# Kernel optimization log

Hardware: AMD Instinct MI355X
Metric: run time of the kernel (lower is better)

Reference implementation:

```python
import jax, jax.numpy as jnp
import numpy as np

DT = 0.1


def setup_inputs() -> dict:
    key = jax.random.key(0)
    k1, k2, k3, k4 = jax.random.split(key, 4)
    B, T, I, H, O = 32, 1024, 256, 512, 256
    return {
        "x": jax.random.normal(k1, (B, T, I), dtype=jnp.float32),
        "input_weights": jax.random.normal(k2, (H, I), dtype=jnp.float32) * (1.0 / np.sqrt(I)),
        "recurrent_weights": jax.random.normal(k3, (H, H), dtype=jnp.float32) * (1.0 / np.sqrt(H)),
        "time_constants": jnp.ones((H,), dtype=jnp.float32) + 0.1,
        "output_weights": jax.random.normal(k4, (O, H), dtype=jnp.float32) * (1.0 / np.sqrt(H)),
        "bias": jnp.zeros((H,), dtype=jnp.float32),
    }


def reference(x, input_weights, recurrent_weights, time_constants, output_weights, bias):
    B = x.shape[0]
    H = recurrent_weights.shape[0]
    h0 = jnp.zeros((B, H), dtype=x.dtype)

    # Precompute the input projection for all timesteps at once: (B,T,I)@(I,H) -> (T,B,H)
    sensory_all = jnp.einsum("bti,hi->tbh", x, input_weights)

    def step(hidden, sensory):
        # sensory: (B, H)
        recurrent = hidden @ recurrent_weights.T                      # (B, H)
        adaptive_tau = jax.nn.softplus(
            time_constants + 0.1 * jnp.mean(jnp.abs(sensory), axis=0)
        )                                                             # (H,)
        activation = jnp.tanh(sensory + recurrent + bias)             # (B, H)
        dhidden_dt = -hidden / adaptive_tau[None, :] + activation
        hidden = hidden + DT * dhidden_dt
        out_t = hidden @ output_weights.T                             # (B, O)
        return hidden, out_t

    final_hidden, outputs = jax.lax.scan(step, h0, sensory_all)        # outputs: (T, B, O)
    output = jnp.transpose(outputs, (1, 0, 2))                          # (B, T, O)
    return output, final_hidden
```

## Files before the change

kernel.cpp:

```cpp
#include <hip/hip_runtime.h>
#include <cstddef>
#include <cstdint>

#define B_ 32
#define T_ 1024
#define IN_ 256
#define H_ 512
#define O_ 256
#define DT_ 0.1f

typedef _Float16 half2_t __attribute__((ext_vector_type(2)));

__device__ __forceinline__ float fdot2(half2_t a, half2_t b, float c) {
    return __builtin_amdgcn_fdot2(a, b, c, false);
}
__device__ __forceinline__ half2_t cvt2(float x, float y) {
    half2_t r; r[0] = (_Float16)x; r[1] = (_Float16)y; return r;
}
__device__ __forceinline__ half2_t as_h2(float f) {
    union { float f; half2_t h; } u; u.f = f; return u.h;
}

template<int N, int K, bool SWA, bool SWC>
__global__ __launch_bounds__(256, 4) void gemm128(const float* __restrict__ A,
                                                  const float* __restrict__ Bw,
                                                  float* __restrict__ C) {
    __shared__ float al[32][132];
    __shared__ float bl[32][132];
    const int tid = threadIdx.x;
    const int m0 = blockIdx.x * 128;
    const int n0 = blockIdx.y * 128;
    const int tx = tid & 15;
    const int ty = tid >> 4;
    float acc[8][8] = {};

    const int lrow = tid >> 3;
    const int kk = (tid & 7) * 4;

    for (int kc = 0; kc < K; kc += 32) {
        __syncthreads();
#pragma unroll
        for (int p = 0; p < 4; ++p) {
            const int row = lrow + p * 32;
            const int m = m0 + row;
            const size_t aoff = SWA ? ((size_t)((m & 31) * T_ + (m >> 5)) * K)
                                    : ((size_t)m * K);
            const float4 v = *(const float4*)(A + aoff + kc + kk);
            al[kk + 0][row] = v.x; al[kk + 1][row] = v.y;
            al[kk + 2][row] = v.z; al[kk + 3][row] = v.w;
        }
#pragma unroll
        for (int p = 0; p < 4; ++p) {
            const int row = lrow + p * 32;
            const float4 v = *(const float4*)(Bw + (size_t)(n0 + row) * K + kc + kk);
            bl[kk + 0][row] = v.x; bl[kk + 1][row] = v.y;
            bl[kk + 2][row] = v.z; bl[kk + 3][row] = v.w;
        }
        __syncthreads();
#pragma unroll
        for (int k = 0; k < 32; ++k) {
            float av[8], bv[8];
            *(float4*)&av[0] = *(const float4*)&al[k][ty * 8];
            *(float4*)&av[4] = *(const float4*)&al[k][ty * 8 + 4];
            *(float4*)&bv[0] = *(const float4*)&bl[k][tx * 8];
            *(float4*)&bv[4] = *(const float4*)&bl[k][tx * 8 + 4];
#pragma unroll
            for (int i = 0; i < 8; ++i)
#pragma unroll
                for (int j = 0; j < 8; ++j)
                    acc[i][j] = fmaf(av[i], bv[j], acc[i][j]);
        }
    }
#pragma unroll
    for (int i = 0; i < 8; ++i) {
        const int m = m0 + ty * 8 + i;
        const size_t coff = SWC ? ((size_t)((m & 31) * T_ + (m >> 5)) * N)
                                : ((size_t)m * N);
        const float4 v0 = make_float4(acc[i][0], acc[i][1], acc[i][2], acc[i][3]);
        const float4 v1 = make_float4(acc[i][4], acc[i][5], acc[i][6], acc[i][7]);
        *(float4*)(C + coff + n0 + tx * 8) = v0;
        *(float4*)(C + coff + n0 + tx * 8 + 4) = v1;
    }
}

__global__ __launch_bounds__(512) void tau_kernel(const float* __restrict__ sens,
                                                  const float* __restrict__ tc,
                                                  float* __restrict__ acoef) {
    const int t = blockIdx.x;
    const int h = threadIdx.x;
    float s = 0.f;
#pragma unroll 8
    for (int b = 0; b < B_; ++b)
        s += fabsf(sens[((size_t)t * B_ + b) * H_ + h]);
    const float x = tc[h] + 0.1f * (s * (1.f / 32.f));
    const float sp = fmaxf(x, 0.f) + log1pf(expf(-fabsf(x)));
    acoef[(size_t)t * H_ + h] = 1.f - DT_ / sp;
}

#define LDSW_BYTES (16 * 512 * 16)
#define SMEM_P     (4 * 512 * 4)
#define SMEM_TOT   (LDSW_BYTES + SMEM_P + 1024)

#define LW(r, p) (*(const float4*)(wl + ((size_t)((r) * 4 + (p)) * 512 + tid) * 4))
#define BARRIER_LGKM() asm volatile("s_waitcnt lgkmcnt(0)\n\ts_barrier" ::: "memory")

__global__ __attribute__((amdgpu_flat_work_group_size(512, 512),
                          amdgpu_waves_per_eu(2, 2), amdgpu_num_vgpr(256)))
void scan_kernel(const float* __restrict__ Wr, const float* __restrict__ acoef,
                 const float* __restrict__ bias, float* sensH,
                 float* __restrict__ finalh) {
    extern __shared__ char smem[];
    half2_t* wl   = (half2_t*)smem;
    float* pred   = (float*)(smem + LDSW_BYTES);
    _Float16* h2s = (_Float16*)(smem + LDSW_BYTES + SMEM_P);

    const int tid  = threadIdx.x;
    const int b    = blockIdx.x;
    const int lane = tid & 63;
    const int w    = tid >> 6;
    const int cw   = w & 3;
    const int rh   = w >> 2;
    const int row0 = rh * 256 + lane * 4;
    const int col0 = cw * 128;

    half2_t wr[4][48];
#pragma unroll
    for (int r = 0; r < 4; ++r) {
        const float* wrow = Wr + (size_t)(row0 + r) * H_ + col0;
#pragma unroll
        for (int k = 0; k < 48; ++k) {
            const float2 v = *(const float2*)(wrow + 2 * k);
            wr[r][k] = cvt2(v.x, v.y);
        }
#pragma unroll
        for (int pp = 0; pp < 4; ++pp)
#pragma unroll
            for (int j = 0; j < 4; ++j) {
                const int k = 48 + pp * 4 + j;
                const float2 v = *(const float2*)(wrow + 2 * k);
                wl[((size_t)(r * 4 + pp) * 512 + tid) * 4 + j] = cvt2(v.x, v.y);
            }
    }

    if (tid < 256) ((half2_t*)h2s)[tid] = cvt2(0.f, 0.f);
    float h_reg = 0.f;
    const float bias_r = bias[tid];
    float s_cur = sensH[(size_t)b * H_ + tid];
    float a_cur = acoef[tid];
    __syncthreads();

    const half2_t* h2c = (const half2_t*)h2s + cw * 64;

    for (int t = 0; t < T_; ++t) {
        const int tn = (t < T_ - 1) ? t + 1 : t;
        const float s_nxt = sensH[((size_t)tn * B_ + b) * H_ + tid];
        const float a_nxt = acoef[(size_t)tn * H_ + tid];

        float acc[4]  = {0.f, 0.f, 0.f, 0.f};
        float accB[4] = {0.f, 0.f, 0.f, 0.f};

        float4 hb0 = *(const float4*)(h2c + 0);
        float4 hb1 = *(const float4*)(h2c + 4);
#pragma unroll
        for (int bt = 0; bt < 6; ++bt) {
            const int nx = (bt < 5) ? 8 * (bt + 1) : 0;
            const float4 nb0 = *(const float4*)(h2c + nx);
            const float4 nb1 = *(const float4*)(h2c + nx + 4);
            const half2_t hh[8] = {as_h2(hb0.x), as_h2(hb0.y), as_h2(hb0.z), as_h2(hb0.w),
                                   as_h2(hb1.x), as_h2(hb1.y), as_h2(hb1.z), as_h2(hb1.w)};
#pragma unroll
            for (int j = 0; j < 8; ++j) {
                const int k = bt * 8 + j;
                acc[0] = fdot2(wr[0][k], hh[j], acc[0]);
                acc[1] = fdot2(wr[1][k], hh[j], acc[1]);
                acc[2] = fdot2(wr[2][k], hh[j], acc[2]);
                acc[3] = fdot2(wr[3][k], hh[j], acc[3]);
            }
            hb0 = nb0; hb1 = nb1;
        }

        {
            const float4 t0 = *(const float4*)(h2c + 48);
            const float4 t1 = *(const float4*)(h2c + 52);
            const float4 t2 = *(const float4*)(h2c + 56);
            const float4 t3 = *(const float4*)(h2c + 60);
            const half2_t ht[16] = {as_h2(t0.x), as_h2(t0.y), as_h2(t0.z), as_h2(t0.w),
                                    as_h2(t1.x), as_h2(t1.y), as_h2(t1.z), as_h2(t1.w),
                                    as_h2(t2.x), as_h2(t2.y), as_h2(t2.z), as_h2(t2.w),
                                    as_h2(t3.x), as_h2(t3.y), as_h2(t3.z), as_h2(t3.w)};
#pragma unroll
            for (int r = 0; r < 4; ++r) {
                const float4 w0 = LW(r, 0), w1 = LW(r, 1);
                acc[r]  = fdot2(as_h2(w0.x), ht[0], acc[r]);
                accB[r] = fdot2(as_h2(w0.y), ht[1], accB[r]);
                acc[r]  = fdot2(as_h2(w0.z), ht[2], acc[r]);
                accB[r] = fdot2(as_h2(w0.w), ht[3], accB[r]);
                acc[r]  = fdot2(as_h2(w1.x), ht[4], acc[r]);
                accB[r] = fdot2(as_h2(w1.y), ht[5], accB[r]);
                acc[r]  = fdot2(as_h2(w1.z), ht[6], acc[r]);
                accB[r] = fdot2(as_h2(w1.w), ht[7], accB[r]);
                const float4 w2 = LW(r, 2), w3 = LW(r, 3);
                acc[r]  = fdot2(as_h2(w2.x), ht[8],  acc[r]);
                accB[r] = fdot2(as_h2(w2.y), ht[9],  accB[r]);
                acc[r]  = fdot2(as_h2(w2.z), ht[10], acc[r]);
                accB[r] = fdot2(as_h2(w2.w), ht[11], accB[r]);
                acc[r]  = fdot2(as_h2(w3.x), ht[12], acc[r]);
                accB[r] = fdot2(as_h2(w3.y), ht[13], accB[r]);
                acc[r]  = fdot2(as_h2(w3.z), ht[14], acc[r]);
                accB[r] = fdot2(as_h2(w3.w), ht[15], accB[r]);
            }
        }

        *(float4*)(pred + cw * 512 + row0) =
            make_float4(acc[0] + accB[0], acc[1] + accB[1],
                        acc[2] + accB[2], acc[3] + accB[3]);
        BARRIER_LGKM();

        {
            const float rec = pred[tid] + pred[512 + tid] +
                              pred[1024 + tid] + pred[1536 + tid];
            const float act = tanhf(s_cur + rec + bias_r);
            h_reg = a_cur * h_reg + DT_ * act;
            sensH[((size_t)t * B_ + b) * H_ + tid] = h_reg;
            h2s[tid] = (_Float16)h_reg;
            s_cur = s_nxt;
            a_cur = a_nxt;
        }
        BARRIER_LGKM();
    }
    finalh[(size_t)b * H_ + tid] = h_reg;
}

extern "C" void kernel_launch(void* const* d_in, const int* in_sizes, int n_in,
                              void* d_out, int out_size, void* d_ws, size_t ws_size,
                              hipStream_t stream) {
    const float* x    = (const float*)d_in[0];
    const float* Win  = (const float*)d_in[1];
    const float* Wr   = (const float*)d_in[2];
    const float* tc   = (const float*)d_in[3];
    const float* Wo   = (const float*)d_in[4];
    const float* bias = (const float*)d_in[5];
    float* out = (float*)d_out;

    float* sensH = (float*)d_ws;
    float* acoef = sensH + (size_t)T_ * B_ * H_;
    const size_t need = ((size_t)T_ * B_ * H_ + (size_t)T_ * H_) * sizeof(float);
    if (ws_size < need) return;

    (void)hipFuncSetAttribute((const void*)scan_kernel,
                              hipFuncAttributeMaxDynamicSharedMemorySize, SMEM_TOT);

    {
        dim3 grid(32768 / 128, H_ / 128);
        hipLaunchKernelGGL((gemm128<H_, IN_, true, false>), grid, dim3(256), 0, stream,
                           x, Win, sensH);
    }
    hipLaunchKernelGGL(tau_kernel, dim3(T_), dim3(H_), 0, stream, sensH, tc, acoef);
    hipLaunchKernelGGL(scan_kernel, dim3(B_), dim3(512), SMEM_TOT, stream,
                       Wr, acoef, bias, sensH, out + (size_t)B_ * T_ * O_);
    {
        dim3 grid(32768 / 128, O_ / 128);
        hipLaunchKernelGGL((gemm128<O_, H_, false, true>), grid, dim3(256), 0, stream,
                           sensH, Wo, out);
    }
}
```

Before: 1.798 ms.

## Compute recurrent matvec with MFMA 16x16x32 f16 instead of fdot2

Replaces the per-thread fdot2 recurrent matrix-vector product with MFMA 16x16x32 f16 instructions. Each wave now owns 64 full rows over the whole K range, so the four-way cross-wave partial-sum reduction through LDS disappears. Three quarters of the weights stay in registers as f16x8 fragments and the last quarter sits in LDS. Because the hidden vector is broadcast across all 16 MFMA columns, most of the matrix-unit work is redundant, but the per-step dependent latency and the LDS reduction traffic should shrink.

Result: slower. 2.147 ms (+19.4%).

```diff
diff --git a/kernel.cpp b/kernel.cpp
--- a/kernel.cpp
+++ b/kernel.cpp
@@ -9,17 +9,8 @@
 #define O_ 256
 #define DT_ 0.1f
 
-typedef _Float16 half2_t __attribute__((ext_vector_type(2)));
-
-__device__ __forceinline__ float fdot2(half2_t a, half2_t b, float c) {
-    return __builtin_amdgcn_fdot2(a, b, c, false);
-}
-__device__ __forceinline__ half2_t cvt2(float x, float y) {
-    half2_t r; r[0] = (_Float16)x; r[1] = (_Float16)y; return r;
-}
-__device__ __forceinline__ half2_t as_h2(float f) {
-    union { float f; half2_t h; } u; u.f = f; return u.h;
-}
+typedef _Float16 f16x8 __attribute__((ext_vector_type(8)));
+typedef float f32x4 __attribute__((ext_vector_type(4)));
 
 template<int N, int K, bool SWA, bool SWC>
 __global__ __launch_bounds__(256, 4) void gemm128(const float* __restrict__ A,
@@ -97,128 +88,118 @@
     acoef[(size_t)t * H_ + h] = 1.f - DT_ / sp;
 }
 
-#define LDSW_BYTES (16 * 512 * 16)
-#define SMEM_P     (4 * 512 * 4)
-#define SMEM_TOT   (LDSW_BYTES + SMEM_P + 1024)
-
-#define LW(r, p) (*(const float4*)(wl + ((size_t)((r) * 4 + (p)) * 512 + tid) * 4))
+#define WLDS_BYTES 131072
+#define PRED_OFF   WLDS_BYTES
+#define H2S_OFF    (WLDS_BYTES + 2048)
+#define SMEM_TOT   (WLDS_BYTES + 2048 + 1024)
+
 #define BARRIER_LGKM() asm volatile("s_waitcnt lgkmcnt(0)\n\ts_barrier" ::: "memory")
+#define MFMA16(a, b, c) __builtin_amdgcn_mfma_f32_16x16x32_f16(a, b, c, 0, 0, 0)
 
 __global__ __attribute__((amdgpu_flat_work_group_size(512, 512),
-                          amdgpu_waves_per_eu(2, 2), amdgpu_num_vgpr(256)))
+                          amdgpu_waves_per_eu(2, 2)))
 void scan_kernel(const float* __restrict__ Wr, const float* __restrict__ acoef,
                  const float* __restrict__ bias, float* sensH,
                  float* __restrict__ finalh) {
     extern __shared__ char smem[];
-    half2_t* wl   = (half2_t*)smem;
-    float* pred   = (float*)(smem + LDSW_BYTES);
-    _Float16* h2s = (_Float16*)(smem + LDSW_BYTES + SMEM_P);
+    float* pred   = (float*)(smem + PRED_OFF);
+    _Float16* h2s = (_Float16*)(smem + H2S_OFF);
 
     const int tid  = threadIdx.x;
     const int b    = blockIdx.x;
     const int lane = tid & 63;
     const int w    = tid >> 6;
-    const int cw   = w & 3;
-    const int rh   = w >> 2;
-    const int row0 = rh * 256 + lane * 4;
-    const int col0 = cw * 128;
-
-    half2_t wr[4][48];
-#pragma unroll
-    for (int r = 0; r < 4; ++r) {
-        const float* wrow = Wr + (size_t)(row0 + r) * H_ + col0;
-#pragma unroll
-        for (int k = 0; k < 48; ++k) {
-            const float2 v = *(const float2*)(wrow + 2 * k);
-            wr[r][k] = cvt2(v.x, v.y);
-        }
-#pragma unroll
-        for (int pp = 0; pp < 4; ++pp)
-#pragma unroll
-            for (int j = 0; j < 4; ++j) {
-                const int k = 48 + pp * 4 + j;
-                const float2 v = *(const float2*)(wrow + 2 * k);
-                wl[((size_t)(r * 4 + pp) * 512 + tid) * 4 + j] = cvt2(v.x, v.y);
+    const int lm   = lane & 15;
+    const int lq   = lane >> 4;
+
+    f16x8 wf0[12], wf1[12], wf2[12], wf3[12];
+#pragma unroll
+    for (int kt = 0; kt < 16; ++kt) {
+#pragma unroll
+        for (int rt = 0; rt < 4; ++rt) {
+            const int row  = w * 64 + rt * 16 + lm;
+            const int col0 = kt * 32 + lq * 8;
+            const float* p = Wr + (size_t)row * H_ + col0;
+            const float4 v0 = *(const float4*)p;
+            const float4 v1 = *(const float4*)(p + 4);
+            f16x8 f;
+            f[0] = (_Float16)v0.x; f[1] = (_Float16)v0.y;
+            f[2] = (_Float16)v0.z; f[3] = (_Float16)v0.w;
+            f[4] = (_Float16)v1.x; f[5] = (_Float16)v1.y;
+            f[6] = (_Float16)v1.z; f[7] = (_Float16)v1.w;
+            if (kt < 12) {
+                if      (rt == 0) wf0[kt] = f;
+                else if (rt == 1) wf1[kt] = f;
+                else if (rt == 2) wf2[kt] = f;
+                else              wf3[kt] = f;
+            } else {
+                *(f16x8*)(smem + ((((kt - 12) * 8 + w) * 4 + rt) * 64 + lane) * 16) = f;
             }
-    }
-
-    if (tid < 256) ((half2_t*)h2s)[tid] = cvt2(0.f, 0.f);
+        }
+    }
+
+    if (tid < 256) ((float*)h2s)[tid] = 0.f;
     float h_reg = 0.f;
     const float bias_r = bias[tid];
     float s_cur = sensH[(size_t)b * H_ + tid];
     float a_cur = acoef[tid];
     __syncthreads();
 
-    const half2_t* h2c = (const half2_t*)h2s + cw * 64;
+    const int bq_base = H2S_OFF + lq * 16;
+    const int wl_base = (w * 4 * 64 + lane) * 16;
+
+#define LDB(kt) (*(const f16x8*)(smem + bq_base + (kt) * 64))
+#define LDW(kt, rt) (*(const f16x8*)(smem + ((kt) - 12) * 32768 + wl_base + (rt) * 1024))
 
     for (int t = 0; t < T_; ++t) {
         const int tn = (t < T_ - 1) ? t + 1 : t;
         const float s_nxt = sensH[((size_t)tn * B_ + b) * H_ + tid];
         const float a_nxt = acoef[(size_t)tn * H_ + tid];
 
-        float acc[4]  = {0.f, 0.f, 0.f, 0.f};
-        float accB[4] = {0.f, 0.f, 0.f, 0.f};
-
-        float4 hb0 = *(const float4*)(h2c + 0);
-        float4 hb1 = *(const float4*)(h2c + 4);
-#pragma unroll
-        for (int bt = 0; bt < 6; ++bt) {
-            const int nx = (bt < 5) ? 8 * (bt + 1) : 0;
-            const float4 nb0 = *(const float4*)(h2c + nx);
-            const float4 nb1 = *(const float4*)(h2c + nx + 4);
-            const half2_t hh[8] = {as_h2(hb0.x), as_h2(hb0.y), as_h2(hb0.z), as_h2(hb0.w),
-                                   as_h2(hb1.x), as_h2(hb1.y), as_h2(hb1.z), as_h2(hb1.w)};
-#pragma unroll
-            for (int j = 0; j < 8; ++j) {
-                const int k = bt * 8 + j;
-                acc[0] = fdot2(wr[0][k], hh[j], acc[0]);
-                acc[1] = fdot2(wr[1][k], hh[j], acc[1]);
-                acc[2] = fdot2(wr[2][k], hh[j], acc[2]);
-                acc[3] = fdot2(wr[3][k], hh[j], acc[3]);
+        f32x4 D0 = {0.f, 0.f, 0.f, 0.f};
+        f32x4 D1 = {0.f, 0.f, 0.f, 0.f};
+        f32x4 D2 = {0.f, 0.f, 0.f, 0.f};
+        f32x4 D3 = {0.f, 0.f, 0.f, 0.f};
+
+        f16x8 bcur = LDB(0);
+#pragma unroll
+        for (int kt = 0; kt < 12; ++kt) {
+            const f16x8 bnxt = LDB(kt + 1);
+            D0 = MFMA16(wf0[kt], bcur, D0);
+            D1 = MFMA16(wf1[kt], bcur, D1);
+            D2 = MFMA16(wf2[kt], bcur, D2);
+            D3 = MFMA16(wf3[kt], bcur, D3);
+            bcur = bnxt;
+        }
+        {
+            f16x8 u0 = LDW(12, 0), u1 = LDW(12, 1), u2 = LDW(12, 2), u3 = LDW(12, 3);
+#pragma unroll
+            for (int kt = 12; kt < 16; ++kt) {
+                f16x8 n0, n1, n2, n3, bnxt;
+                if (kt < 15) {
+                    bnxt = LDB(kt + 1);
+                    n0 = LDW(kt + 1, 0); n1 = LDW(kt + 1, 1);
+                    n2 = LDW(kt + 1, 2); n3 = LDW(kt + 1, 3);
+                }
+                D0 = MFMA16(u0, bcur, D0);
+                D1 = MFMA16(u1, bcur, D1);
+                D2 = MFMA16(u2, bcur, D2);
+                D3 = MFMA16(u3, bcur, D3);
+                if (kt < 15) { u0 = n0; u1 = n1; u2 = n2; u3 = n3; bcur = bnxt; }
             }
-            hb0 = nb0; hb1 = nb1;
-        }
+        }
+
+        if (lm == 0) {
+            float* pb = pred + w * 64 + lq * 4;
+            *(f32x4*)(pb +  0) = D0;
+            *(f32x4*)(pb + 16) = D1;
+            *(f32x4*)(pb + 32) = D2;
+            *(f32x4*)(pb + 48) = D3;
+        }
+        BARRIER_LGKM();
 
         {
-            const float4 t0 = *(const float4*)(h2c + 48);
-            const float4 t1 = *(const float4*)(h2c + 52);
-            const float4 t2 = *(const float4*)(h2c + 56);
-            const float4 t3 = *(const float4*)(h2c + 60);
-            const half2_t ht[16] = {as_h2(t0.x), as_h2(t0.y), as_h2(t0.z), as_h2(t0.w),
-                                    as_h2(t1.x), as_h2(t1.y), as_h2(t1.z), as_h2(t1.w),
-                                    as_h2(t2.x), as_h2(t2.y), as_h2(t2.z), as_h2(t2.w),
-                                    as_h2(t3.x), as_h2(t3.y), as_h2(t3.z), as_h2(t3.w)};
-#pragma unroll
-            for (int r = 0; r < 4; ++r) {
-                const float4 w0 = LW(r, 0), w1 = LW(r, 1);
-                acc[r]  = fdot2(as_h2(w0.x), ht[0], acc[r]);
-                accB[r] = fdot2(as_h2(w0.y), ht[1], accB[r]);
-                acc[r]  = fdot2(as_h2(w0.z), ht[2], acc[r]);
-                accB[r] = fdot2(as_h2(w0.w), ht[3], accB[r]);
-                acc[r]  = fdot2(as_h2(w1.x), ht[4], acc[r]);
-                accB[r] = fdot2(as_h2(w1.y), ht[5], accB[r]);
-                acc[r]  = fdot2(as_h2(w1.z), ht[6], acc[r]);
-                accB[r] = fdot2(as_h2(w1.w), ht[7], accB[r]);
-                const float4 w2 = LW(r, 2), w3 = LW(r, 3);
-                acc[r]  = fdot2(as_h2(w2.x), ht[8],  acc[r]);
-                accB[r] = fdot2(as_h2(w2.y), ht[9],  accB[r]);
-                acc[r]  = fdot2(as_h2(w2.z), ht[10], acc[r]);
-                accB[r] = fdot2(as_h2(w2.w), ht[11], accB[r]);
-                acc[r]  = fdot2(as_h2(w3.x), ht[12], acc[r]);
-                accB[r] = fdot2(as_h2(w3.y), ht[13], accB[r]);
-                acc[r]  = fdot2(as_h2(w3.z), ht[14], acc[r]);
-                accB[r] = fdot2(as_h2(w3.w), ht[15], accB[r]);
-            }
-        }
-
-        *(float4*)(pred + cw * 512 + row0) =
-            make_float4(acc[0] + accB[0], acc[1] + accB[1],
-                        acc[2] + accB[2], acc[3] + accB[3]);
-        BARRIER_LGKM();
-
-        {
-            const float rec = pred[tid] + pred[512 + tid] +
-                              pred[1024 + tid] + pred[1536 + tid];
+            const float rec = pred[tid];
             const float act = tanhf(s_cur + rec + bias_r);
             h_reg = a_cur * h_reg + DT_ * act;
             sensH[((size_t)t * B_ + b) * H_ + tid] = h_reg;
@@ -229,6 +210,8 @@
         BARRIER_LGKM();
     }
     finalh[(size_t)b * H_ + tid] = h_reg;
+#undef LDB
+#undef LDW
 }
 
 extern "C" void kernel_launch(void* const* d_in, const int* in_sizes, int n_in,
```
